# Kernel optimization log

Hardware: AMD Instinct MI355X
Metric: run time of the kernel (lower is better)

The kernel has to match this reference:

```python
import jax, jax.numpy as jnp
import numpy as np

N_NODES = 50000
N_EDGES = 800000
D = 128


def setup_inputs() -> dict:
    key = jax.random.key(0)
    ks = jax.random.split(key, 8)
    std = 1.0 / np.sqrt(D)
    inp = {
        "features": jax.random.normal(ks[0], (N_NODES, D), dtype=jnp.float32),
        "edge_index": jax.random.randint(ks[1], (2, N_EDGES), 0, N_NODES, dtype=jnp.int64),
        "w1a": jax.random.normal(ks[2], (D, D), dtype=jnp.float32) * std,
        "b1a": jnp.zeros((D,), dtype=jnp.float32),
        "w1b": jax.random.normal(ks[3], (D, D), dtype=jnp.float32) * std,
        "b1b": jnp.zeros((D,), dtype=jnp.float32),
        "eps1": jnp.float32(0.0),
        "w2a": jax.random.normal(ks[4], (D, D), dtype=jnp.float32) * std,
        "b2a": jnp.zeros((D,), dtype=jnp.float32),
        "w2b": jax.random.normal(ks[5], (D, D), dtype=jnp.float32) * std,
        "b2b": jnp.zeros((D,), dtype=jnp.float32),
        "eps2": jnp.float32(0.0),
    }
    return inp


def _gin_conv(x, edge_index, wA, bA, wB, bB, eps):
    # GIN: h_i = MLP((1+eps)*x_i + sum_{j in N(i)} x_j)
    src, dst = edge_index[0], edge_index[1]
    agg = jax.ops.segment_sum(x[src], dst, num_segments=x.shape[0])  # [N, D]
    h = (1.0 + eps) * x + agg
    h = jax.nn.relu(h @ wA.T + bA) @ wB.T + bB  # Linear -> ReLU -> Linear
    return h


def reference(features, edge_index, w1a, b1a, w1b, b1b, eps1,
              w2a, b2a, w2b, b2b, eps2):
    x = jax.nn.relu(_gin_conv(features, edge_index, w1a, b1a, w1b, b1b, eps1))
    # F.dropout with training=False (eval mode) is identity
    x = _gin_conv(x, edge_index, w2a, b2a, w2b, b2b, eps2)
    return x
```

## Files before the change

### kernel.cpp

```cpp
#include <hip/hip_runtime.h>
#include <hip/hip_bf16.h>
#include <stddef.h>

#define NN 50000
#define EE 800000
#define DDIM 128
#define CAP 64

#define CAST_BLOCKS 3125
#define WCONV_BLOCKS 32
#define CNTZ_BLOCKS 196
#define PREP_BLOCKS (CAST_BLOCKS + WCONV_BLOCKS + CNTZ_BLOCKS + 1)

typedef short bf16x8 __attribute__((ext_vector_type(8)));
typedef float f32x4  __attribute__((ext_vector_type(4)));

__device__ __forceinline__ float bf2f(unsigned short u) {
  union { unsigned int i; float f; } v; v.i = ((unsigned int)u) << 16; return v.f;
}
__device__ __forceinline__ unsigned short f2bf(float f) {
  __hip_bfloat16 h = __float2bfloat16(f);
  return *reinterpret_cast<unsigned short*>(&h);
}
__device__ __forceinline__ uint4 pack8(const float4 a, const float4 b) {
  uint4 o;
  o.x = f2bf(a.x) | ((unsigned)f2bf(a.y) << 16);
  o.y = f2bf(a.z) | ((unsigned)f2bf(a.w) << 16);
  o.z = f2bf(b.x) | ((unsigned)f2bf(b.y) << 16);
  o.w = f2bf(b.z) | ((unsigned)f2bf(b.w) << 16);
  return o;
}

__global__ __launch_bounds__(256) void k_prep(const float* __restrict__ feat,
                                              const float* __restrict__ w1a,
                                              const float* __restrict__ w1b,
                                              const float* __restrict__ w2a,
                                              const float* __restrict__ w2b,
                                              unsigned short* __restrict__ Xb,
                                              unsigned short* __restrict__ W16,
                                              int* __restrict__ cnt,
                                              unsigned int* __restrict__ zrow)
{
  const int b = blockIdx.x, tid = threadIdx.x;
  if (b < CAST_BLOCKS) {
    int t = b * 256 + tid;
    const float4* p = reinterpret_cast<const float4*>(feat) + (size_t)t * 2;
    reinterpret_cast<uint4*>(Xb)[t] = pack8(p[0], p[1]);
  } else if (b < CAST_BLOCKS + WCONV_BLOCKS) {
    int i = (b - CAST_BLOCKS) * 256 + tid;
    int which = i >> 11, off = i & 2047;
    const float* wp = (which == 0) ? w1a : (which == 1) ? w1b : (which == 2) ? w2a : w2b;
    const float4* p = reinterpret_cast<const float4*>(wp + off * 8);
    reinterpret_cast<uint4*>(W16 + which * 16384)[off] = pack8(p[0], p[1]);
  } else if (b < CAST_BLOCKS + WCONV_BLOCKS + CNTZ_BLOCKS) {
    int i = (b - CAST_BLOCKS - WCONV_BLOCKS) * 256 + tid;
    if (i < NN) cnt[i] = 0;
  } else {
    if (tid < 64) zrow[tid] = 0u;
  }
}

__global__ __launch_bounds__(256) void k_fill(const int* __restrict__ src,
                                              const int* __restrict__ dst,
                                              int* __restrict__ cnt,
                                              int* __restrict__ csr)
{
  int t = blockIdx.x * 256 + threadIdx.x;
  if (t >= EE / 4) return;
  int4 s4 = reinterpret_cast<const int4*>(src)[t];
  int4 d4 = reinterpret_cast<const int4*>(dst)[t];
  int p;
  p = atomicAdd(&cnt[d4.x], 1); csr[(d4.x << 6) + p] = s4.x;
  p = atomicAdd(&cnt[d4.y], 1); csr[(d4.y << 6) + p] = s4.y;
  p = atomicAdd(&cnt[d4.z], 1); csr[(d4.z << 6) + p] = s4.z;
  p = atomicAdd(&cnt[d4.w], 1); csr[(d4.w << 6) + p] = s4.w;
}

__global__ __launch_bounds__(256) void k_gin_agg(const unsigned short* __restrict__ Xb,
                                                 const int* __restrict__ cnt,
                                                 const int* __restrict__ csr,
                                                 const float* __restrict__ eps,
                                                 const unsigned short* __restrict__ zrow,
                                                 unsigned short* __restrict__ Ab)
{
  int node = blockIdx.x * 4 + (threadIdx.x >> 6);
  if (node >= NN) return;
  const int lane = threadIdx.x & 63;
  const int g = lane >> 4;
  const int c = lane & 15;

  float acc[8];
  #pragma unroll
  for (int k = 0; k < 8; ++k) acc[k] = 0.f;

  const int beg = node << 6;
  const int end = beg + cnt[node];
  for (int e = beg; e < end; e += 16) {
    uint4 v[4];
    #pragma unroll
    for (int k = 0; k < 4; ++k) {
      int ee = e + g + 4 * k;
      const unsigned short* prow = (ee < end) ? (Xb + (size_t)csr[ee] * DDIM) : zrow;
      v[k] = *reinterpret_cast<const uint4*>(prow + c * 8);
    }
    __builtin_amdgcn_sched_barrier(0);
    #pragma unroll
    for (int k = 0; k < 4; ++k) {
      acc[0] += bf2f((unsigned short)(v[k].x & 0xffff));
      acc[1] += bf2f((unsigned short)(v[k].x >> 16));
      acc[2] += bf2f((unsigned short)(v[k].y & 0xffff));
      acc[3] += bf2f((unsigned short)(v[k].y >> 16));
      acc[4] += bf2f((unsigned short)(v[k].z & 0xffff));
      acc[5] += bf2f((unsigned short)(v[k].z >> 16));
      acc[6] += bf2f((unsigned short)(v[k].w & 0xffff));
      acc[7] += bf2f((unsigned short)(v[k].w >> 16));
    }
  }

  #pragma unroll
  for (int k = 0; k < 8; ++k) acc[k] += __shfl_xor(acc[k], 16, 64);
  #pragma unroll
  for (int k = 0; k < 8; ++k) acc[k] += __shfl_xor(acc[k], 32, 64);

  const float s = 1.0f + eps[0];
  uint4 sv = *reinterpret_cast<const uint4*>(Xb + (size_t)node * DDIM + c * 8);
  acc[0] += s * bf2f((unsigned short)(sv.x & 0xffff));
  acc[1] += s * bf2f((unsigned short)(sv.x >> 16));
  acc[2] += s * bf2f((unsigned short)(sv.y & 0xffff));
  acc[3] += s * bf2f((unsigned short)(sv.y >> 16));
  acc[4] += s * bf2f((unsigned short)(sv.z & 0xffff));
  acc[5] += s * bf2f((unsigned short)(sv.z >> 16));
  acc[6] += s * bf2f((unsigned short)(sv.w & 0xffff));
  acc[7] += s * bf2f((unsigned short)(sv.w >> 16));

  if (g == 0) {
    uint4 o;
    o.x = f2bf(acc[0]) | ((unsigned)f2bf(acc[1]) << 16);
    o.y = f2bf(acc[2]) | ((unsigned)f2bf(acc[3]) << 16);
    o.z = f2bf(acc[4]) | ((unsigned)f2bf(acc[5]) << 16);
    o.w = f2bf(acc[6]) | ((unsigned)f2bf(acc[7]) << 16);
    *reinterpret_cast<uint4*>(Ab + (size_t)node * DDIM + c * 8) = o;
  }
}

template<int RELU_OUT, int BF16_OUT>
__global__ __launch_bounds__(512) void k_mlp(const unsigned short* __restrict__ Xb,
                                             const unsigned short* __restrict__ Wa16,
                                             const float* __restrict__ Ba,
                                             const unsigned short* __restrict__ Wb16,
                                             const float* __restrict__ Bb,
                                             void* __restrict__ Yout)
{
  __shared__ unsigned short WL[128 * 128];
  __shared__ unsigned short HL[128 * 128];
  const int tid = threadIdx.x;
  const int row0 = blockIdx.x * 128;

  #pragma unroll
  for (int i = 0; i < 4; ++i) {
    int g = tid + i * 512;
    int n = g >> 4, c8 = g & 15;
    uint4 o = reinterpret_cast<const uint4*>(Wa16)[g];
    *reinterpret_cast<uint4*>(&WL[n * 128 + ((c8 ^ (n & 15)) * 8)]) = o;
  }
  __syncthreads();

  const int w = tid >> 6, lane = tid & 63;
  const int m = lane & 15, q = lane >> 4;

  f32x4 acc[8];
  #pragma unroll
  for (int nt = 0; nt < 8; ++nt) acc[nt] = (f32x4){0.f, 0.f, 0.f, 0.f};

  int arow = row0 + w * 16 + m;
  if (arow >= NN) arow = NN - 1;
  const unsigned short* abase = Xb + (size_t)arow * DDIM + q * 8;
  #pragma unroll
  for (int ks = 0; ks < 4; ++ks) {
    bf16x8 a = *reinterpret_cast<const bf16x8*>(abase + ks * 32);
    #pragma unroll
    for (int nt = 0; nt < 8; ++nt) {
      int n = nt * 16 + m;
      bf16x8 b = *reinterpret_cast<const bf16x8*>(&WL[n * 128 + (((ks * 4 + q) ^ (n & 15)) * 8)]);
      acc[nt] = __builtin_amdgcn_mfma_f32_16x16x32_bf16(a, b, acc[nt], 0, 0, 0);
    }
  }

  #pragma unroll
  for (int nt = 0; nt < 8; ++nt) {
    int col = nt * 16 + m;
    float bias = Ba[col];
    #pragma unroll
    for (int reg = 0; reg < 4; ++reg) {
      float v = fmaxf(acc[nt][reg] + bias, 0.f);
      int hrow = w * 16 + q * 4 + reg;
      HL[hrow * 128 + ((((col >> 3) ^ (hrow & 15)) << 3) + (col & 7))] = f2bf(v);
    }
  }
  __syncthreads();

  #pragma unroll
  for (int i = 0; i < 4; ++i) {
    int g = tid + i * 512;
    int n = g >> 4, c8 = g & 15;
    uint4 o = reinterpret_cast<const uint4*>(Wb16)[g];
    *reinterpret_cast<uint4*>(&WL[n * 128 + ((c8 ^ (n & 15)) * 8)]) = o;
  }
  __syncthreads();

  f32x4 acc2[8];
  #pragma unroll
  for (int nt = 0; nt < 8; ++nt) acc2[nt] = (f32x4){0.f, 0.f, 0.f, 0.f};

  const int hrowA = w * 16 + m;
  #pragma unroll
  for (int ks = 0; ks < 4; ++ks) {
    bf16x8 a = *reinterpret_cast<const bf16x8*>(&HL[hrowA * 128 + (((ks * 4 + q) ^ (hrowA & 15)) * 8)]);
    #pragma unroll
    for (int nt = 0; nt < 8; ++nt) {
      int n = nt * 16 + m;
      bf16x8 b = *reinterpret_cast<const bf16x8*>(&WL[n * 128 + (((ks * 4 + q) ^ (n & 15)) * 8)]);
      acc2[nt] = __builtin_amdgcn_mfma_f32_16x16x32_bf16(a, b, acc2[nt], 0, 0, 0);
    }
  }

  #pragma unroll
  for (int nt = 0; nt < 8; ++nt) {
    int col = nt * 16 + m;
    float bias = Bb[col];
    #pragma unroll
    for (int reg = 0; reg < 4; ++reg) {
      int grow = row0 + w * 16 + q * 4 + reg;
      if (grow >= NN) continue;
      float v = acc2[nt][reg] + bias;
      if (RELU_OUT) v = fmaxf(v, 0.f);
      if (BF16_OUT)
        reinterpret_cast<unsigned short*>(Yout)[(size_t)grow * DDIM + col] = f2bf(v);
      else
        reinterpret_cast<float*>(Yout)[(size_t)grow * DDIM + col] = v;
    }
  }
}

extern "C" void kernel_launch(void* const* d_in, const int* in_sizes, int n_in,
                              void* d_out, int out_size, void* d_ws, size_t ws_size,
                              hipStream_t stream)
{
  const float* feat = (const float*)d_in[0];
  const int*   ei   = (const int*)d_in[1];
  const float* w1a  = (const float*)d_in[2];
  const float* b1a  = (const float*)d_in[3];
  const float* w1b  = (const float*)d_in[4];
  const float* b1b  = (const float*)d_in[5];
  const float* eps1 = (const float*)d_in[6];
  const float* w2a  = (const float*)d_in[7];
  const float* b2a  = (const float*)d_in[8];
  const float* w2b  = (const float*)d_in[9];
  const float* b2b  = (const float*)d_in[10];
  const float* eps2 = (const float*)d_in[11];
  float* out = (float*)d_out;

  const int* src = ei;
  const int* dst = ei + EE;

  char* w = (char*)d_ws;
  unsigned short* zrow = (unsigned short*)w;  w += 256;
  int* cnt  = (int*)w;                        w += ((NN * 4 + 255) & ~255);
  int* csr  = (int*)w;                        w += (((size_t)NN * CAP * 4 + 255) & ~255);
  unsigned short* W16 = (unsigned short*)w;   w += ((4 * 128 * 128 * 2 + 255) & ~255);
  unsigned short* Xb = (unsigned short*)w;    w += ((size_t)NN * DDIM * 2 + 255) & ~255;
  unsigned short* Ab = (unsigned short*)w;    w += ((size_t)NN * DDIM * 2 + 255) & ~255;

  const unsigned short* W1a16 = W16;
  const unsigned short* W1b16 = W16 + 16384;
  const unsigned short* W2a16 = W16 + 2 * 16384;
  const unsigned short* W2b16 = W16 + 3 * 16384;

  const int fill_blocks = (EE / 4 + 255) / 256;
  const int agg_blocks  = (NN + 3) / 4;
  const int mlp_blocks  = (NN + 127) / 128;

  k_prep<<<PREP_BLOCKS, 256, 0, stream>>>(feat, w1a, w1b, w2a, w2b, Xb, W16, cnt,
                                          (unsigned int*)zrow);
  k_fill<<<fill_blocks, 256, 0, stream>>>(src, dst, cnt, csr);

  k_gin_agg<<<agg_blocks, 256, 0, stream>>>(Xb, cnt, csr, eps1, zrow, Ab);
  k_mlp<1, 1><<<mlp_blocks, 512, 0, stream>>>(Ab, W1a16, b1a, W1b16, b1b, (void*)Xb);

  k_gin_agg<<<agg_blocks, 256, 0, stream>>>(Xb, cnt, csr, eps2, zrow, Ab);
  k_mlp<0, 0><<<mlp_blocks, 512, 0, stream>>>(Ab, W2a16, b2a, W2b16, b2b, (void*)out);
}
```

Before: 245.4 us.

## Fuse GIN aggregation into MLP kernel and merge CSR fill into prep

Each GIN layer now runs as one kernel: 512-thread blocks gather neighbor rows for their 128 nodes into shared memory, then run both MLP matmuls on that tile. This removes the aggregated intermediate's global write and read, plus two launches. The CSR fill is folded into the prep kernel, and count zeroing moves to a memset issued before it, so the fill still sees zeroed counts. The cost is 391 large blocks with one wave per 16 nodes doing serial gathers, which lowers gather parallelism and occupancy compared with the small standalone aggregation blocks.

```diff
diff --git a/kernel.cpp b/kernel.cpp
--- a/kernel.cpp
+++ b/kernel.cpp
@@ -9,8 +9,8 @@
 
 #define CAST_BLOCKS 3125
 #define WCONV_BLOCKS 32
-#define CNTZ_BLOCKS 196
-#define PREP_BLOCKS (CAST_BLOCKS + WCONV_BLOCKS + CNTZ_BLOCKS + 1)
+#define FILL_BLOCKS 782
+#define PREP_BLOCKS (CAST_BLOCKS + WCONV_BLOCKS + FILL_BLOCKS)
 
 typedef short bf16x8 __attribute__((ext_vector_type(8)));
 typedef float f32x4  __attribute__((ext_vector_type(4)));
@@ -36,10 +36,12 @@
                                               const float* __restrict__ w1b,
                                               const float* __restrict__ w2a,
                                               const float* __restrict__ w2b,
+                                              const int* __restrict__ src,
+                                              const int* __restrict__ dst,
                                               unsigned short* __restrict__ Xb,
                                               unsigned short* __restrict__ W16,
                                               int* __restrict__ cnt,
-                                              unsigned int* __restrict__ zrow)
+                                              int* __restrict__ csr)
 {
   const int b = blockIdx.x, tid = threadIdx.x;
   if (b < CAST_BLOCKS) {
@@ -52,137 +54,121 @@
     const float* wp = (which == 0) ? w1a : (which == 1) ? w1b : (which == 2) ? w2a : w2b;
     const float4* p = reinterpret_cast<const float4*>(wp + off * 8);
     reinterpret_cast<uint4*>(W16 + which * 16384)[off] = pack8(p[0], p[1]);
-  } else if (b < CAST_BLOCKS + WCONV_BLOCKS + CNTZ_BLOCKS) {
-    int i = (b - CAST_BLOCKS - WCONV_BLOCKS) * 256 + tid;
-    if (i < NN) cnt[i] = 0;
   } else {
-    if (tid < 64) zrow[tid] = 0u;
-  }
-}
-
-__global__ __launch_bounds__(256) void k_fill(const int* __restrict__ src,
-                                              const int* __restrict__ dst,
-                                              int* __restrict__ cnt,
-                                              int* __restrict__ csr)
+    int t = (b - CAST_BLOCKS - WCONV_BLOCKS) * 256 + tid;
+    if (t < EE / 4) {
+      int4 s4 = reinterpret_cast<const int4*>(src)[t];
+      int4 d4 = reinterpret_cast<const int4*>(dst)[t];
+      int p;
+      p = atomicAdd(&cnt[d4.x], 1); csr[(d4.x << 6) + p] = s4.x;
+      p = atomicAdd(&cnt[d4.y], 1); csr[(d4.y << 6) + p] = s4.y;
+      p = atomicAdd(&cnt[d4.z], 1); csr[(d4.z << 6) + p] = s4.z;
+      p = atomicAdd(&cnt[d4.w], 1); csr[(d4.w << 6) + p] = s4.w;
+    }
+  }
+}
+
+template<int RELU_OUT, int BF16_OUT>
+__global__ __launch_bounds__(512) void k_fused(const unsigned short* __restrict__ Xin,
+                                               const int* __restrict__ cnt,
+                                               const int* __restrict__ csr,
+                                               const float* __restrict__ eps,
+                                               const unsigned short* __restrict__ zrow,
+                                               const unsigned short* __restrict__ Wa16,
+                                               const float* __restrict__ Ba,
+                                               const unsigned short* __restrict__ Wb16,
+                                               const float* __restrict__ Bb,
+                                               void* __restrict__ Yout)
 {
-  int t = blockIdx.x * 256 + threadIdx.x;
-  if (t >= EE / 4) return;
-  int4 s4 = reinterpret_cast<const int4*>(src)[t];
-  int4 d4 = reinterpret_cast<const int4*>(dst)[t];
-  int p;
-  p = atomicAdd(&cnt[d4.x], 1); csr[(d4.x << 6) + p] = s4.x;
-  p = atomicAdd(&cnt[d4.y], 1); csr[(d4.y << 6) + p] = s4.y;
-  p = atomicAdd(&cnt[d4.z], 1); csr[(d4.z << 6) + p] = s4.z;
-  p = atomicAdd(&cnt[d4.w], 1); csr[(d4.w << 6) + p] = s4.w;
-}
-
-__global__ __launch_bounds__(256) void k_gin_agg(const unsigned short* __restrict__ Xb,
-                                                 const int* __restrict__ cnt,
-                                                 const int* __restrict__ csr,
-                                                 const float* __restrict__ eps,
-                                                 const unsigned short* __restrict__ zrow,
-                                                 unsigned short* __restrict__ Ab)
-{
-  int node = blockIdx.x * 4 + (threadIdx.x >> 6);
-  if (node >= NN) return;
-  const int lane = threadIdx.x & 63;
+  __shared__ unsigned short WL[128 * 128];
+  __shared__ unsigned short AH[128 * 128];
+  const int tid = threadIdx.x;
+  const int row0 = blockIdx.x * 128;
+  const int w = tid >> 6, lane = tid & 63;
   const int g = lane >> 4;
   const int c = lane & 15;
 
-  float acc[8];
-  #pragma unroll
-  for (int k = 0; k < 8; ++k) acc[k] = 0.f;
-
-  const int beg = node << 6;
-  const int end = beg + cnt[node];
-  for (int e = beg; e < end; e += 16) {
-    uint4 v[4];
-    #pragma unroll
-    for (int k = 0; k < 4; ++k) {
-      int ee = e + g + 4 * k;
-      const unsigned short* prow = (ee < end) ? (Xb + (size_t)csr[ee] * DDIM) : zrow;
-      v[k] = *reinterpret_cast<const uint4*>(prow + c * 8);
-    }
-    __builtin_amdgcn_sched_barrier(0);
-    #pragma unroll
-    for (int k = 0; k < 4; ++k) {
-      acc[0] += bf2f((unsigned short)(v[k].x & 0xffff));
-      acc[1] += bf2f((unsigned short)(v[k].x >> 16));
-      acc[2] += bf2f((unsigned short)(v[k].y & 0xffff));
-      acc[3] += bf2f((unsigned short)(v[k].y >> 16));
-      acc[4] += bf2f((unsigned short)(v[k].z & 0xffff));
-      acc[5] += bf2f((unsigned short)(v[k].z >> 16));
-      acc[6] += bf2f((unsigned short)(v[k].w & 0xffff));
-      acc[7] += bf2f((unsigned short)(v[k].w >> 16));
-    }
-  }
-
-  #pragma unroll
-  for (int k = 0; k < 8; ++k) acc[k] += __shfl_xor(acc[k], 16, 64);
-  #pragma unroll
-  for (int k = 0; k < 8; ++k) acc[k] += __shfl_xor(acc[k], 32, 64);
+  #pragma unroll
+  for (int i = 0; i < 4; ++i) {
+    int gi = tid + i * 512;
+    int n = gi >> 4, c8 = gi & 15;
+    uint4 o = reinterpret_cast<const uint4*>(Wa16)[gi];
+    *reinterpret_cast<uint4*>(&WL[n * 128 + ((c8 ^ (n & 15)) * 8)]) = o;
+  }
 
   const float s = 1.0f + eps[0];
-  uint4 sv = *reinterpret_cast<const uint4*>(Xb + (size_t)node * DDIM + c * 8);
-  acc[0] += s * bf2f((unsigned short)(sv.x & 0xffff));
-  acc[1] += s * bf2f((unsigned short)(sv.x >> 16));
-  acc[2] += s * bf2f((unsigned short)(sv.y & 0xffff));
-  acc[3] += s * bf2f((unsigned short)(sv.y >> 16));
-  acc[4] += s * bf2f((unsigned short)(sv.z & 0xffff));
-  acc[5] += s * bf2f((unsigned short)(sv.z >> 16));
-  acc[6] += s * bf2f((unsigned short)(sv.w & 0xffff));
-  acc[7] += s * bf2f((unsigned short)(sv.w >> 16));
-
-  if (g == 0) {
-    uint4 o;
-    o.x = f2bf(acc[0]) | ((unsigned)f2bf(acc[1]) << 16);
-    o.y = f2bf(acc[2]) | ((unsigned)f2bf(acc[3]) << 16);
-    o.z = f2bf(acc[4]) | ((unsigned)f2bf(acc[5]) << 16);
-    o.w = f2bf(acc[6]) | ((unsigned)f2bf(acc[7]) << 16);
-    *reinterpret_cast<uint4*>(Ab + (size_t)node * DDIM + c * 8) = o;
-  }
-}
-
-template<int RELU_OUT, int BF16_OUT>
-__global__ __launch_bounds__(512) void k_mlp(const unsigned short* __restrict__ Xb,
-                                             const unsigned short* __restrict__ Wa16,
-                                             const float* __restrict__ Ba,
-                                             const unsigned short* __restrict__ Wb16,
-                                             const float* __restrict__ Bb,
-                                             void* __restrict__ Yout)
-{
-  __shared__ unsigned short WL[128 * 128];
-  __shared__ unsigned short HL[128 * 128];
-  const int tid = threadIdx.x;
-  const int row0 = blockIdx.x * 128;
-
-  #pragma unroll
-  for (int i = 0; i < 4; ++i) {
-    int g = tid + i * 512;
-    int n = g >> 4, c8 = g & 15;
-    uint4 o = reinterpret_cast<const uint4*>(Wa16)[g];
-    *reinterpret_cast<uint4*>(&WL[n * 128 + ((c8 ^ (n & 15)) * 8)]) = o;
+  for (int i = 0; i < 16; ++i) {
+    const int hrow = w * 16 + i;
+    const int node = row0 + hrow;
+    if (node < NN) {
+      float acc[8];
+      #pragma unroll
+      for (int k = 0; k < 8; ++k) acc[k] = 0.f;
+      const int beg = node << 6;
+      const int end = beg + cnt[node];
+      for (int e = beg; e < end; e += 16) {
+        uint4 v[4];
+        #pragma unroll
+        for (int k = 0; k < 4; ++k) {
+          int ee = e + g + 4 * k;
+          const unsigned short* prow = (ee < end) ? (Xin + (size_t)csr[ee] * DDIM) : zrow;
+          v[k] = *reinterpret_cast<const uint4*>(prow + c * 8);
+        }
+        __builtin_amdgcn_sched_barrier(0);
+        #pragma unroll
+        for (int k = 0; k < 4; ++k) {
+          acc[0] += bf2f((unsigned short)(v[k].x & 0xffff));
+          acc[1] += bf2f((unsigned short)(v[k].x >> 16));
+          acc[2] += bf2f((unsigned short)(v[k].y & 0xffff));
+          acc[3] += bf2f((unsigned short)(v[k].y >> 16));
+          acc[4] += bf2f((unsigned short)(v[k].z & 0xffff));
+          acc[5] += bf2f((unsigned short)(v[k].z >> 16));
+          acc[6] += bf2f((unsigned short)(v[k].w & 0xffff));
+          acc[7] += bf2f((unsigned short)(v[k].w >> 16));
+        }
+      }
+      #pragma unroll
+      for (int k = 0; k < 8; ++k) acc[k] += __shfl_xor(acc[k], 16, 64);
+      #pragma unroll
+      for (int k = 0; k < 8; ++k) acc[k] += __shfl_xor(acc[k], 32, 64);
+      uint4 sv = *reinterpret_cast<const uint4*>(Xin + (size_t)node * DDIM + c * 8);
+      acc[0] += s * bf2f((unsigned short)(sv.x & 0xffff));
+      acc[1] += s * bf2f((unsigned short)(sv.x >> 16));
+      acc[2] += s * bf2f((unsigned short)(sv.y & 0xffff));
+      acc[3] += s * bf2f((unsigned short)(sv.y >> 16));
+      acc[4] += s * bf2f((unsigned short)(sv.z & 0xffff));
+      acc[5] += s * bf2f((unsigned short)(sv.z >> 16));
+      acc[6] += s * bf2f((unsigned short)(sv.w & 0xffff));
+      acc[7] += s * bf2f((unsigned short)(sv.w >> 16));
+      if (g == 0) {
+        uint4 o;
+        o.x = f2bf(acc[0]) | ((unsigned)f2bf(acc[1]) << 16);
+        o.y = f2bf(acc[2]) | ((unsigned)f2bf(acc[3]) << 16);
+        o.z = f2bf(acc[4]) | ((unsigned)f2bf(acc[5]) << 16);
+        o.w = f2bf(acc[6]) | ((unsigned)f2bf(acc[7]) << 16);
+        *reinterpret_cast<uint4*>(&AH[hrow * 128 + ((c ^ (hrow & 15)) * 8)]) = o;
+      }
+    } else if (g == 0) {
+      uint4 z = make_uint4(0u, 0u, 0u, 0u);
+      *reinterpret_cast<uint4*>(&AH[hrow * 128 + ((c ^ (hrow & 15)) * 8)]) = z;
+    }
   }
   __syncthreads();
 
-  const int w = tid >> 6, lane = tid & 63;
   const int m = lane & 15, q = lane >> 4;
 
-  f32x4 acc[8];
-  #pragma unroll
-  for (int nt = 0; nt < 8; ++nt) acc[nt] = (f32x4){0.f, 0.f, 0.f, 0.f};
-
-  int arow = row0 + w * 16 + m;
-  if (arow >= NN) arow = NN - 1;
-  const unsigned short* abase = Xb + (size_t)arow * DDIM + q * 8;
+  f32x4 acc1[8];
+  #pragma unroll
+  for (int nt = 0; nt < 8; ++nt) acc1[nt] = (f32x4){0.f, 0.f, 0.f, 0.f};
+  const int hrowA = w * 16 + m;
   #pragma unroll
   for (int ks = 0; ks < 4; ++ks) {
-    bf16x8 a = *reinterpret_cast<const bf16x8*>(abase + ks * 32);
+    bf16x8 a = *reinterpret_cast<const bf16x8*>(&AH[hrowA * 128 + (((ks * 4 + q) ^ m) * 8)]);
     #pragma unroll
     for (int nt = 0; nt < 8; ++nt) {
       int n = nt * 16 + m;
       bf16x8 b = *reinterpret_cast<const bf16x8*>(&WL[n * 128 + (((ks * 4 + q) ^ (n & 15)) * 8)]);
-      acc[nt] = __builtin_amdgcn_mfma_f32_16x16x32_bf16(a, b, acc[nt], 0, 0, 0);
+      acc1[nt] = __builtin_amdgcn_mfma_f32_16x16x32_bf16(a, b, acc1[nt], 0, 0, 0);
     }
   }
 
@@ -192,18 +178,18 @@
     float bias = Ba[col];
     #pragma unroll
     for (int reg = 0; reg < 4; ++reg) {
-      float v = fmaxf(acc[nt][reg] + bias, 0.f);
+      float v = fmaxf(acc1[nt][reg] + bias, 0.f);
       int hrow = w * 16 + q * 4 + reg;
-      HL[hrow * 128 + ((((col >> 3) ^ (hrow & 15)) << 3) + (col & 7))] = f2bf(v);
+      AH[hrow * 128 + ((((col >> 3) ^ (hrow & 15)) << 3) + (col & 7))] = f2bf(v);
     }
   }
   __syncthreads();
 
   #pragma unroll
   for (int i = 0; i < 4; ++i) {
-    int g = tid + i * 512;
-    int n = g >> 4, c8 = g & 15;
-    uint4 o = reinterpret_cast<const uint4*>(Wb16)[g];
+    int gi = tid + i * 512;
+    int n = gi >> 4, c8 = gi & 15;
+    uint4 o = reinterpret_cast<const uint4*>(Wb16)[gi];
     *reinterpret_cast<uint4*>(&WL[n * 128 + ((c8 ^ (n & 15)) * 8)]) = o;
   }
   __syncthreads();
@@ -211,11 +197,9 @@
   f32x4 acc2[8];
   #pragma unroll
   for (int nt = 0; nt < 8; ++nt) acc2[nt] = (f32x4){0.f, 0.f, 0.f, 0.f};
-
-  const int hrowA = w * 16 + m;
   #pragma unroll
   for (int ks = 0; ks < 4; ++ks) {
-    bf16x8 a = *reinterpret_cast<const bf16x8*>(&HL[hrowA * 128 + (((ks * 4 + q) ^ (hrowA & 15)) * 8)]);
+    bf16x8 a = *reinterpret_cast<const bf16x8*>(&AH[hrowA * 128 + (((ks * 4 + q) ^ m) * 8)]);
     #pragma unroll
     for (int nt = 0; nt < 8; ++nt) {
       int n = nt * 16 + m;
@@ -269,24 +253,21 @@
   int* csr  = (int*)w;                        w += (((size_t)NN * CAP * 4 + 255) & ~255);
   unsigned short* W16 = (unsigned short*)w;   w += ((4 * 128 * 128 * 2 + 255) & ~255);
   unsigned short* Xb = (unsigned short*)w;    w += ((size_t)NN * DDIM * 2 + 255) & ~255;
-  unsigned short* Ab = (unsigned short*)w;    w += ((size_t)NN * DDIM * 2 + 255) & ~255;
+  unsigned short* X1 = (unsigned short*)w;    w += ((size_t)NN * DDIM * 2 + 255) & ~255;
 
   const unsigned short* W1a16 = W16;
   const unsigned short* W1b16 = W16 + 16384;
   const unsigned short* W2a16 = W16 + 2 * 16384;
   const unsigned short* W2b16 = W16 + 3 * 16384;
 
-  const int fill_blocks = (EE / 4 + 255) / 256;
-  const int agg_blocks  = (NN + 3) / 4;
-  const int mlp_blocks  = (NN + 127) / 128;
-
-  k_prep<<<PREP_BLOCKS, 256, 0, stream>>>(feat, w1a, w1b, w2a, w2b, Xb, W16, cnt,
-                                          (unsigned int*)zrow);
-  k_fill<<<fill_blocks, 256, 0, stream>>>(src, dst, cnt, csr);
-
-  k_gin_agg<<<agg_blocks, 256, 0, stream>>>(Xb, cnt, csr, eps1, zrow, Ab);
-  k_mlp<1, 1><<<mlp_blocks, 512, 0, stream>>>(Ab, W1a16, b1a, W1b16, b1b, (void*)Xb);
-
-  k_gin_agg<<<agg_blocks, 256, 0, stream>>>(Xb, cnt, csr, eps2, zrow, Ab);
-  k_mlp<0, 0><<<mlp_blocks, 512, 0, stream>>>(Ab, W2a16, b2a, W2b16, b2b, (void*)out);
-}
+  const int fused_blocks = (NN + 127) / 128;
+
+  hipMemsetAsync(zrow, 0, 256 + NN * sizeof(int), stream);
+  k_prep<<<PREP_BLOCKS, 256, 0, stream>>>(feat, w1a, w1b, w2a, w2b, src, dst,
+                                          Xb, W16, cnt, csr);
+
+  k_fused<1, 1><<<fused_blocks, 512, 0, stream>>>(Xb, cnt, csr, eps1, zrow,
+                                                  W1a16, b1a, W1b16, b1b, (void*)X1);
+  k_fused<0, 0><<<fused_blocks, 512, 0, stream>>>(X1, cnt, csr, eps2, zrow,
+                                                  W2a16, b2a, W2b16, b2b, (void*)out);
+}
```

Result: slower. 280.1 us (+14.1%).
